# Performance work log

Hardware: AMD Instinct MI355X
Metric: run time of the kernel (lower is better)

Reference implementation:

```python
import jax, jax.numpy as jnp
import numpy as np

N_NODES = 50000
N_EDGES = 800000
N_REL = 8
DIM = 256


def setup_inputs() -> dict:
    key = jax.random.key(0)
    ks = jax.random.split(key, 6)
    x = jax.random.normal(ks[0], (N_NODES, DIM), dtype=jnp.float32)
    # xavier-uniform-ish scale for [R, in, out] weights
    limit = float(np.sqrt(6.0 / (DIM + DIM)))
    W0 = jax.random.uniform(ks[1], (N_REL, DIM, DIM), dtype=jnp.float32, minval=-limit, maxval=limit)
    W1 = jax.random.uniform(ks[2], (N_REL, DIM, DIM), dtype=jnp.float32, minval=-limit, maxval=limit)
    b0 = jnp.zeros((DIM,), dtype=jnp.float32)
    b1 = jnp.zeros((DIM,), dtype=jnp.float32)
    edge_index = jax.random.randint(ks[3], (2, N_EDGES), 0, N_NODES, dtype=jnp.int64)
    edge_type = jax.random.randint(ks[4], (N_EDGES,), 0, N_REL, dtype=jnp.int64)
    return {"x": x, "W0": W0, "b0": b0, "W1": W1, "b1": b1,
            "edge_index": edge_index, "edge_type": edge_type}


def _rgcn_layer(x, W, b, src, dst, edge_type, num_nodes):
    # grouped GEMM over all relations: [R, N, out]
    xt = jnp.einsum('ni,rio->rno', x, W)
    # per-edge message = relu(x[src] @ W[edge_type] + b)  -> [E, out]
    msg = jax.nn.relu(xt[edge_type, src] + b)
    # scatter-add into destination nodes
    return jax.ops.segment_sum(msg, dst, num_segments=num_nodes)


def reference(x, W0, b0, W1, b1, edge_index, edge_type):
    src, dst = edge_index[0], edge_index[1]
    h = _rgcn_layer(x, W0, b0, src, dst, edge_type, x.shape[0])
    h = _rgcn_layer(h, W1, b1, src, dst, edge_type, x.shape[0])
    return h
```

## Files before the change

kernel.cpp:

```cpp
#include <hip/hip_runtime.h>

#define DIM 256
#define N_REL 8

typedef __attribute__((ext_vector_type(8))) short short8_t;
typedef __attribute__((ext_vector_type(4))) float float4_t;

__device__ inline unsigned short f2bf(float f) {
    unsigned u = __float_as_uint(f);
    u += 0x7FFFu + ((u >> 16) & 1u);
    return (unsigned short)(u >> 16);
}
__device__ inline float bf2f(unsigned short h) {
    return __uint_as_float(((unsigned)h) << 16);
}

__global__ __launch_bounds__(256) void cast_f32_bf16(
    const float* __restrict__ in, unsigned short* __restrict__ out, int n4)
{
    const int i = blockIdx.x * blockDim.x + threadIdx.x;
    if (i >= n4) return;
    const float4 v = ((const float4*)in)[i];
    ushort4 o;
    o.x = f2bf(v.x); o.y = f2bf(v.y); o.z = f2bf(v.z); o.w = f2bf(v.w);
    ((ushort4*)out)[i] = o;
}

__global__ __launch_bounds__(256) void transpose_cast_w(
    const float* __restrict__ W, unsigned short* __restrict__ Wt)
{
    __shared__ float tile[32][33];
    const int rel = blockIdx.z;
    const int i0 = blockIdx.x * 32, o0 = blockIdx.y * 32;
    const int tx = threadIdx.x, ty = threadIdx.y;
    const float* Wr = W + (size_t)rel * DIM * DIM;
    unsigned short* Wtr = Wt + (size_t)rel * DIM * DIM;
#pragma unroll
    for (int j = 0; j < 4; j++)
        tile[ty + 8 * j][tx] = Wr[(size_t)(i0 + ty + 8 * j) * DIM + o0 + tx];
    __syncthreads();
#pragma unroll
    for (int j = 0; j < 4; j++)
        Wtr[(size_t)(o0 + ty + 8 * j) * DIM + i0 + tx] = f2bf(tile[tx][ty + 8 * j]);
}

__global__ __launch_bounds__(256) void gemm_mfma_bias_relu(
    const unsigned short* __restrict__ Xb,
    const unsigned short* __restrict__ Wtb,
    const float* __restrict__ bias,
    unsigned short* __restrict__ Yall, int M, int Rtiles)
{
    __shared__ __align__(16) short smem[10240];
    short* As = smem;
    short* Bs = smem + 5120;

    const unsigned L = blockIdx.x;
    const int xcd = L & 7;
    const unsigned g = L >> 3;
    const int combo = g & 15;
    const int rt = (int)((g >> 4) << 3) | xcd;
    if (rt >= Rtiles) return;
    const int m0 = rt * 128;
    const int n0 = (combo & 1) * 128;
    const int rel = combo >> 1;

    const unsigned short* Wt = Wtb + (size_t)rel * DIM * DIM;
    unsigned short* Y = Yall + (size_t)rel * M * DIM;

    const int t = threadIdx.x;
    const int lane = t & 63;
    const int w = t >> 6;
    const int wr = w & 1, wc = w >> 1;
    const int r = lane & 15, q = lane >> 4;

    const int rowA0 = t >> 2;
    const int segA0 = t & 3;

    float4_t acc[4][4];
#pragma unroll
    for (int i = 0; i < 4; i++)
#pragma unroll
        for (int j = 0; j < 4; j++) {
            float4_t z = {0.f, 0.f, 0.f, 0.f};
            acc[i][j] = z;
        }

    short8_t ra[2], rb[2];
    const short8_t zero8 = {0, 0, 0, 0, 0, 0, 0, 0};

#define LOAD_TILES(ks)                                                            \
    {                                                                             \
        const int k0_ = (ks) * 32;                                                \
        _Pragma("unroll")                                                         \
        for (int h = 0; h < 2; h++) {                                             \
            const int row_ = rowA0 + h * 64;                                      \
            const int m_ = m0 + row_;                                             \
            if (m_ < M)                                                           \
                ra[h] = *(const short8_t*)(Xb + (size_t)m_ * DIM + k0_ + segA0 * 8); \
            else                                                                  \
                ra[h] = zero8;                                                    \
            rb[h] = *(const short8_t*)(Wt + (size_t)(n0 + row_) * DIM + k0_ + segA0 * 8); \
        }                                                                         \
    }

    LOAD_TILES(0);
#pragma unroll 1
    for (int ks = 0; ks < 8; ks++) {
#pragma unroll
        for (int h = 0; h < 2; h++) {
            const int row_ = rowA0 + h * 64;
            *(short8_t*)&As[row_ * 40 + segA0 * 8] = ra[h];
            *(short8_t*)&Bs[row_ * 40 + segA0 * 8] = rb[h];
        }
        __syncthreads();
        if (ks < 7) LOAD_TILES(ks + 1);

        short8_t af[4], bf[4];
#pragma unroll
        for (int mi = 0; mi < 4; mi++)
            af[mi] = *(const short8_t*)&As[(wr * 64 + mi * 16 + r) * 40 + q * 8];
#pragma unroll
        for (int ni = 0; ni < 4; ni++)
            bf[ni] = *(const short8_t*)&Bs[(wc * 64 + ni * 16 + r) * 40 + q * 8];
#pragma unroll
        for (int mi = 0; mi < 4; mi++)
#pragma unroll
            for (int ni = 0; ni < 4; ni++)
                acc[mi][ni] = __builtin_amdgcn_mfma_f32_16x16x32_bf16(
                    af[mi], bf[ni], acc[mi][ni], 0, 0, 0);
        __syncthreads();
    }
#undef LOAD_TILES

    short* St = smem;

    float bv[4];
#pragma unroll
    for (int ni = 0; ni < 4; ni++)
        bv[ni] = bias[n0 + wc * 64 + ni * 16 + r];

#pragma unroll
    for (int mi = 0; mi < 4; mi++) {
#pragma unroll
        for (int ni = 0; ni < 4; ni++) {
#pragma unroll
            for (int e = 0; e < 4; e++) {
                const int rl = wr * 16 + q * 4 + e;
                const int col = wc * 64 + ni * 16 + r;
                St[rl * 136 + col] = f2bf(fmaxf(acc[mi][ni][e] + bv[ni], 0.f));
            }
        }
        __syncthreads();
#pragma unroll
        for (int j = 0; j < 2; j++) {
            const int id = t + 256 * j;
            const int rl = id >> 4;
            const int ch = id & 15;
            const int grow = m0 + (rl >> 4) * 64 + mi * 16 + (rl & 15);
            const short8_t v = *(const short8_t*)&St[rl * 136 + ch * 8];
            if (grow < M)
                *(short8_t*)&Y[(size_t)grow * DIM + n0 + ch * 8] = v;
        }
        __syncthreads();
    }
}

__global__ __launch_bounds__(256) void count_dst(
    const int* __restrict__ dst, int E, int* __restrict__ cnt)
{
    const int e = blockIdx.x * blockDim.x + threadIdx.x;
    if (e < E) atomicAdd(&cnt[dst[e]], 1);
}

__global__ __launch_bounds__(256) void scan_blocksums(
    const int* __restrict__ cnt, int N, int* __restrict__ bsum)
{
    __shared__ int red[256];
    const int t = threadIdx.x;
    const int base = blockIdx.x * 1024 + t * 4;
    int s = 0;
#pragma unroll
    for (int j = 0; j < 4; j++) {
        const int i = base + j;
        if (i < N) s += cnt[i];
    }
    red[t] = s;
    __syncthreads();
#pragma unroll
    for (int off = 128; off > 0; off >>= 1) {
        if (t < off) red[t] += red[t + off];
        __syncthreads();
    }
    if (t == 0) bsum[blockIdx.x] = red[0];
}

__global__ __launch_bounds__(256) void scan_offsets(
    int* __restrict__ bsum, int nb, int* __restrict__ rowptr, int N)
{
    __shared__ int sh[256];
    const int t = threadIdx.x;
    sh[t] = (t < nb) ? bsum[t] : 0;
    __syncthreads();
    for (int off = 1; off < 256; off <<= 1) {
        const int add = (t >= off) ? sh[t - off] : 0;
        __syncthreads();
        sh[t] += add;
        __syncthreads();
    }
    if (t < nb) bsum[t] = (t == 0) ? 0 : sh[t - 1];
    if (t == 255) rowptr[N] = sh[255];
}

__global__ __launch_bounds__(256) void scan_phase3(
    const int* __restrict__ cnt, int N, const int* __restrict__ bsum,
    int* __restrict__ rowptr, int* __restrict__ cursor)
{
    __shared__ int sh[256];
    const int t = threadIdx.x;
    const int base = blockIdx.x * 1024 + t * 4;
    int v[4];
#pragma unroll
    for (int j = 0; j < 4; j++) {
        const int i = base + j;
        v[j] = (i < N) ? cnt[i] : 0;
    }
    sh[t] = v[0] + v[1] + v[2] + v[3];
    __syncthreads();
    for (int off = 1; off < 256; off <<= 1) {
        const int add = (t >= off) ? sh[t - off] : 0;
        __syncthreads();
        sh[t] += add;
        __syncthreads();
    }
    int run = bsum[blockIdx.x] + ((t == 0) ? 0 : sh[t - 1]);
#pragma unroll
    for (int j = 0; j < 4; j++) {
        const int i = base + j;
        if (i < N) { rowptr[i] = run; cursor[i] = run; }
        run += v[j];
    }
}

__global__ __launch_bounds__(256) void fill_edges(
    const int* __restrict__ src, const int* __restrict__ dst,
    const int* __restrict__ et, int E, int* __restrict__ cursor,
    unsigned* __restrict__ ep)
{
    const int e = blockIdx.x * blockDim.x + threadIdx.x;
    if (e >= E) return;
    const int pos = atomicAdd(&cursor[dst[e]], 1);
    ep[pos] = (unsigned)src[e] | ((unsigned)et[e] << 16);
}

template <typename OT>
__global__ __launch_bounds__(256) void aggregate4(
    const unsigned short* __restrict__ yall,
    const unsigned* __restrict__ ep, const int* __restrict__ rowptr,
    OT* __restrict__ out, int M)
{
    const int lane = threadIdx.x & 63;
    const int half = lane >> 5;
    const int cl = lane & 31;
    const int wv = (blockIdx.x * blockDim.x + threadIdx.x) >> 6;
    const int nw = (gridDim.x * blockDim.x) >> 6;
    const size_t plane = (size_t)M * DIM;

    for (int d = wv; d < M; d += nw) {
        const int beg = rowptr[d], end = rowptr[d + 1];
        float acc[8];
#pragma unroll
        for (int j = 0; j < 8; j++) acc[j] = 0.f;

        for (int c0 = beg; c0 < end; c0 += 64) {
            const int n = min(64, end - c0);
            const unsigned myep = (c0 + lane < end) ? ep[c0 + lane] : 0u;
            for (int i = 0; i < n; i += 4) {
                const int i0 = i + half;
                const int i1 = i + 2 + half;
                const unsigned p0 = __shfl(myep, i0 & 63);
                const unsigned p1 = __shfl(myep, i1 & 63);
                const short8_t u0 = *(const short8_t*)(
                    yall + (size_t)(p0 >> 16) * plane +
                    (size_t)(p0 & 0xFFFFu) * DIM + cl * 8);
                const short8_t u1 = *(const short8_t*)(
                    yall + (size_t)(p1 >> 16) * plane +
                    (size_t)(p1 & 0xFFFFu) * DIM + cl * 8);
                if (i0 < n) {
#pragma unroll
                    for (int j = 0; j < 8; j++)
                        acc[j] += bf2f((unsigned short)u0[j]);
                }
                if (i1 < n) {
#pragma unroll
                    for (int j = 0; j < 8; j++)
                        acc[j] += bf2f((unsigned short)u1[j]);
                }
            }
        }
        float o[8];
#pragma unroll
        for (int j = 0; j < 8; j++)
            o[j] = acc[j] + __shfl(acc[j], (lane + 32) & 63);
        if (lane < 32) {
            OT* dp = out + (size_t)d * DIM + cl * 8;
            if (sizeof(OT) == 4) {
                *(float4*)((float*)dp) = make_float4(o[0], o[1], o[2], o[3]);
                *(float4*)((float*)dp + 4) = make_float4(o[4], o[5], o[6], o[7]);
            } else {
                short8_t v;
#pragma unroll
                for (int j = 0; j < 8; j++) v[j] = (short)f2bf(o[j]);
                *(short8_t*)((unsigned short*)dp) = v;
            }
        }
    }
}

__global__ __launch_bounds__(256) void gemm_bias_relu_f32(
    const float* __restrict__ A, const float* __restrict__ B,
    const float* __restrict__ bias, float* __restrict__ Y, int M)
{
    __shared__ float Asf[16][132];
    __shared__ float Bsf[16][128];
    const int t = threadIdx.x;
    const int tx = t & 15, ty = t >> 4;
    const int row0 = blockIdx.x * 128, col0 = blockIdx.y * 128;
    float acc[8][8];
#pragma unroll
    for (int i = 0; i < 8; i++)
#pragma unroll
        for (int j = 0; j < 8; j++) acc[i][j] = 0.f;
    const int arow = t >> 2, akseg = (t & 3) * 4;
    const int bk0 = t >> 5, bcol = (t & 31) * 4;
    for (int k0 = 0; k0 < DIM; k0 += 16) {
#pragma unroll
        for (int h = 0; h < 2; h++) {
            const int row = row0 + arow + h * 64;
            float4 av = (row < M) ? *(const float4*)(A + (size_t)row * DIM + k0 + akseg)
                                  : make_float4(0, 0, 0, 0);
            Asf[akseg + 0][arow + h * 64] = av.x;
            Asf[akseg + 1][arow + h * 64] = av.y;
            Asf[akseg + 2][arow + h * 64] = av.z;
            Asf[akseg + 3][arow + h * 64] = av.w;
        }
#pragma unroll
        for (int h = 0; h < 2; h++) {
            const int krow = bk0 + h * 8;
            *(float4*)&Bsf[krow][bcol] =
                *(const float4*)(B + (size_t)(k0 + krow) * DIM + col0 + bcol);
        }
        __syncthreads();
#pragma unroll
        for (int k = 0; k < 16; k++) {
            float a[8], b[8];
            *(float4*)&a[0] = *(const float4*)&Asf[k][ty * 4];
            *(float4*)&a[4] = *(const float4*)&Asf[k][64 + ty * 4];
            *(float4*)&b[0] = *(const float4*)&Bsf[k][tx * 4];
            *(float4*)&b[4] = *(const float4*)&Bsf[k][64 + tx * 4];
#pragma unroll
            for (int i = 0; i < 8; i++)
#pragma unroll
                for (int j = 0; j < 8; j++) acc[i][j] = fmaf(a[i], b[j], acc[i][j]);
        }
        __syncthreads();
    }
#pragma unroll
    for (int im = 0; im < 2; im++)
#pragma unroll
        for (int i = 0; i < 4; i++) {
            const int row = row0 + im * 64 + ty * 4 + i;
            if (row >= M) continue;
#pragma unroll
            for (int jm = 0; jm < 2; jm++) {
                const int col = col0 + jm * 64 + tx * 4;
                const float4 bb = *(const float4*)(bias + col);
                float4 o;
                o.x = fmaxf(acc[im * 4 + i][jm * 4 + 0] + bb.x, 0.f);
                o.y = fmaxf(acc[im * 4 + i][jm * 4 + 1] + bb.y, 0.f);
                o.z = fmaxf(acc[im * 4 + i][jm * 4 + 2] + bb.z, 0.f);
                o.w = fmaxf(acc[im * 4 + i][jm * 4 + 3] + bb.w, 0.f);
                *(float4*)(Y + (size_t)row * DIM + col) = o;
            }
        }
}

__global__ __launch_bounds__(256) void scatter_rel(
    const float* __restrict__ y, const int* __restrict__ src,
    const int* __restrict__ dst, const int* __restrict__ et,
    int rel, float* __restrict__ out, int n_edges)
{
    const int lane = threadIdx.x & 63;
    const int wave = (blockIdx.x * blockDim.x + threadIdx.x) >> 6;
    const int nwaves = (gridDim.x * blockDim.x) >> 6;
    for (int e = wave; e < n_edges; e += nwaves) {
        if (et[e] != rel) continue;
        const float4 v = *(const float4*)(y + (size_t)src[e] * DIM + lane * 4);
        float* o = out + (size_t)dst[e] * DIM + lane * 4;
        atomicAdd(o + 0, v.x);
        atomicAdd(o + 1, v.y);
        atomicAdd(o + 2, v.z);
        atomicAdd(o + 3, v.w);
    }
}

static inline size_t align16(size_t x) { return (x + 15) & ~(size_t)15; }

extern "C" void kernel_launch(void* const* d_in, const int* in_sizes, int n_in,
                              void* d_out, int out_size, void* d_ws, size_t ws_size,
                              hipStream_t stream)
{
    const float* x  = (const float*)d_in[0];
    const float* W0 = (const float*)d_in[1];
    const float* b0 = (const float*)d_in[2];
    const float* W1 = (const float*)d_in[3];
    const float* b1 = (const float*)d_in[4];
    const int* eidx = (const int*)d_in[5];
    const int* etyp = (const int*)d_in[6];

    const int M = in_sizes[0] / DIM;
    const int E = in_sizes[6];
    const int* src = eidx;
    const int* dst = eidx + E;
    float* out = (float*)d_out;

    const size_t plane = (size_t)M * DIM;
    const size_t wbytes = (size_t)N_REL * DIM * DIM * 2;

    const size_t need = align16(plane * 2)
                      + align16(plane * 2)
                      + 2 * align16(wbytes)
                      + align16((size_t)(M + 1) * 4)
                      + 2 * align16((size_t)M * 4)
                      + align16((size_t)256 * 4)
                      + align16((size_t)E * 4)
                      + align16((size_t)N_REL * plane * 2);

    if (M < 65536 && ws_size >= need) {
        char* ws = (char*)d_ws;
        size_t off = 0;
        unsigned short* h1b  = (unsigned short*)(ws + off); off = align16(off + plane * 2);
        unsigned short* xb   = (unsigned short*)(ws + off); off = align16(off + plane * 2);
        unsigned short* Wt0b = (unsigned short*)(ws + off); off = align16(off + wbytes);
        unsigned short* Wt1b = (unsigned short*)(ws + off); off = align16(off + wbytes);
        int* rowptr = (int*)(ws + off); off = align16(off + (size_t)(M + 1) * 4);
        int* cnt    = (int*)(ws + off); off = align16(off + (size_t)M * 4);
        int* cursor = (int*)(ws + off); off = align16(off + (size_t)M * 4);
        int* bsum   = (int*)(ws + off); off = align16(off + (size_t)256 * 4);
        unsigned* ep = (unsigned*)(ws + off); off = align16(off + (size_t)E * 4);
        unsigned short* yall = (unsigned short*)(ws + off);

        const int nb = (M + 1023) / 1024;
        hipMemsetAsync(cnt, 0, (size_t)M * 4, stream);
        count_dst<<<(E + 255) / 256, 256, 0, stream>>>(dst, E, cnt);
        scan_blocksums<<<nb, 256, 0, stream>>>(cnt, M, bsum);
        scan_offsets<<<1, 256, 0, stream>>>(bsum, nb, rowptr, M);
        scan_phase3<<<nb, 256, 0, stream>>>(cnt, M, bsum, rowptr, cursor);
        fill_edges<<<(E + 255) / 256, 256, 0, stream>>>(src, dst, etyp, E, cursor, ep);

        cast_f32_bf16<<<(int)((plane / 4 + 255) / 256), 256, 0, stream>>>(
            x, xb, (int)(plane / 4));
        transpose_cast_w<<<dim3(8, 8, N_REL), dim3(32, 8), 0, stream>>>(W0, Wt0b);
        transpose_cast_w<<<dim3(8, 8, N_REL), dim3(32, 8), 0, stream>>>(W1, Wt1b);

        const int Rtiles = (M + 127) / 128;
        const int octets = (Rtiles + 7) / 8;
        const int ggrid = octets * 16 * 8;
        const int agrid = (int)(((size_t)M * 64 + 255) / 256);

        gemm_mfma_bias_relu<<<ggrid, 256, 0, stream>>>(xb, Wt0b, b0, yall, M, Rtiles);
        aggregate4<unsigned short><<<agrid, 256, 0, stream>>>(yall, ep, rowptr, h1b, M);
        gemm_mfma_bias_relu<<<ggrid, 256, 0, stream>>>(h1b, Wt1b, b1, yall, M, Rtiles);
        aggregate4<float><<<agrid, 256, 0, stream>>>(yall, ep, rowptr, out, M);
    } else {
        float* h1 = (float*)d_ws;
        float* y  = (float*)d_ws + plane;
        const dim3 gblk(256), ggrid2((M + 127) / 128, DIM / 128);
        hipMemsetAsync(h1, 0, plane * 4, stream);
        for (int r = 0; r < N_REL; r++) {
            gemm_bias_relu_f32<<<ggrid2, gblk, 0, stream>>>(
                x, W0 + (size_t)r * DIM * DIM, b0, y, M);
            scatter_rel<<<1024, 256, 0, stream>>>(y, src, dst, etyp, r, h1, E);
        }
        hipMemsetAsync(out, 0, plane * 4, stream);
        for (int r = 0; r < N_REL; r++) {
            gemm_bias_relu_f32<<<ggrid2, gblk, 0, stream>>>(
                h1, W1 + (size_t)r * DIM * DIM, b1, y, M);
            scatter_rel<<<1024, 256, 0, stream>>>(y, src, dst, etyp, r, out, E);
        }
    }
}
```

Baseline: 538.8 us.

## Double-buffer GEMM tiles via direct global-to-LDS loads with XOR swizzle

The GEMM main loop now stages A/B tiles straight from global memory into LDS using global_load_lds, which skips the register round-trip. Tiles are double-buffered so the next k-slice loads while MFMAs run on the current one. Padded row strides are replaced by an XOR swizzle to avoid LDS bank conflicts. The M-bound check on A rows was dropped, so the last partial row tile may read past the end of X, and synchronisation now relies on hand-written waitcnt and barrier instructions.

```diff
diff --git a/kernel.cpp b/kernel.cpp
--- a/kernel.cpp
+++ b/kernel.cpp
@@ -50,9 +50,7 @@
     const float* __restrict__ bias,
     unsigned short* __restrict__ Yall, int M, int Rtiles)
 {
-    __shared__ __align__(16) short smem[10240];
-    short* As = smem;
-    short* Bs = smem + 5120;
+    __shared__ __align__(16) short smem[16384];
 
     const unsigned L = blockIdx.x;
     const int xcd = L & 7;
@@ -73,8 +71,26 @@
     const int wr = w & 1, wc = w >> 1;
     const int r = lane & 15, q = lane >> 4;
 
-    const int rowA0 = t >> 2;
-    const int segA0 = t & 3;
+    const int sl = lane & 3;
+    const int rsub = lane >> 2;
+    const unsigned short* gA[2];
+    const unsigned short* gB[2];
+#pragma unroll
+    for (int h = 0; h < 2; h++) {
+        const int row = h * 64 + w * 16 + rsub;
+        const int gseg = sl ^ ((row >> 1) & 3);
+        gA[h] = Xb + (size_t)(m0 + row) * DIM + gseg * 8;
+        gB[h] = Wt + (size_t)(n0 + row) * DIM + gseg * 8;
+    }
+
+    const int swz = (q ^ ((r >> 1) & 3)) * 8;
+    int offA[4], offB[4];
+#pragma unroll
+    for (int mi = 0; mi < 4; mi++)
+        offA[mi] = (wr * 64 + mi * 16 + r) * 32 + swz;
+#pragma unroll
+    for (int ni = 0; ni < 4; ni++)
+        offB[ni] = (wc * 64 + ni * 16 + r) * 32 + swz;
 
     float4_t acc[4][4];
 #pragma unroll
@@ -85,52 +101,54 @@
             acc[i][j] = z;
         }
 
-    short8_t ra[2], rb[2];
-    const short8_t zero8 = {0, 0, 0, 0, 0, 0, 0, 0};
-
-#define LOAD_TILES(ks)                                                            \
-    {                                                                             \
-        const int k0_ = (ks) * 32;                                                \
-        _Pragma("unroll")                                                         \
-        for (int h = 0; h < 2; h++) {                                             \
-            const int row_ = rowA0 + h * 64;                                      \
-            const int m_ = m0 + row_;                                             \
-            if (m_ < M)                                                           \
-                ra[h] = *(const short8_t*)(Xb + (size_t)m_ * DIM + k0_ + segA0 * 8); \
-            else                                                                  \
-                ra[h] = zero8;                                                    \
-            rb[h] = *(const short8_t*)(Wt + (size_t)(n0 + row_) * DIM + k0_ + segA0 * 8); \
-        }                                                                         \
-    }
-
-    LOAD_TILES(0);
+#define STAGE(ks, bsel)                                                         \
+    {                                                                           \
+        const int k0_ = (ks) * 32;                                              \
+        short* Ad_ = smem + ((bsel) ? 8192 : 0);                                \
+        short* Bd_ = Ad_ + 4096;                                                \
+        _Pragma("unroll")                                                       \
+        for (int h = 0; h < 2; h++) {                                           \
+            __builtin_amdgcn_global_load_lds(                                   \
+                (const __attribute__((address_space(1))) unsigned int*)(gA[h] + k0_), \
+                (__attribute__((address_space(3))) unsigned int*)(Ad_ + h * 2048 + w * 512), \
+                16, 0, 0);                                                      \
+            __builtin_amdgcn_global_load_lds(                                   \
+                (const __attribute__((address_space(1))) unsigned int*)(gB[h] + k0_), \
+                (__attribute__((address_space(3))) unsigned int*)(Bd_ + h * 2048 + w * 512), \
+                16, 0, 0);                                                      \
+        }                                                                       \
+    }
+
+    STAGE(0, 0);
 #pragma unroll 1
     for (int ks = 0; ks < 8; ks++) {
-#pragma unroll
-        for (int h = 0; h < 2; h++) {
-            const int row_ = rowA0 + h * 64;
-            *(short8_t*)&As[row_ * 40 + segA0 * 8] = ra[h];
-            *(short8_t*)&Bs[row_ * 40 + segA0 * 8] = rb[h];
-        }
-        __syncthreads();
-        if (ks < 7) LOAD_TILES(ks + 1);
-
+        const int cur = ks & 1;
+        if (ks < 7) {
+            STAGE(ks + 1, cur ^ 1);
+            asm volatile("s_waitcnt vmcnt(4)" ::: "memory");
+        } else {
+            asm volatile("s_waitcnt vmcnt(0)" ::: "memory");
+        }
+        asm volatile("s_barrier" ::: "memory");
+
+        const short* As_b = smem + (cur ? 8192 : 0);
+        const short* Bs_b = As_b + 4096;
         short8_t af[4], bf[4];
 #pragma unroll
         for (int mi = 0; mi < 4; mi++)
-            af[mi] = *(const short8_t*)&As[(wr * 64 + mi * 16 + r) * 40 + q * 8];
+            af[mi] = *(const short8_t*)&As_b[offA[mi]];
 #pragma unroll
         for (int ni = 0; ni < 4; ni++)
-            bf[ni] = *(const short8_t*)&Bs[(wc * 64 + ni * 16 + r) * 40 + q * 8];
+            bf[ni] = *(const short8_t*)&Bs_b[offB[ni]];
 #pragma unroll
         for (int mi = 0; mi < 4; mi++)
 #pragma unroll
             for (int ni = 0; ni < 4; ni++)
                 acc[mi][ni] = __builtin_amdgcn_mfma_f32_16x16x32_bf16(
                     af[mi], bf[ni], acc[mi][ni], 0, 0, 0);
-        __syncthreads();
-    }
-#undef LOAD_TILES
+        asm volatile("s_barrier" ::: "memory");
+    }
+#undef STAGE
 
     short* St = smem;
 
```

After: 510.0 us. -5.4%, faster.
